# Kernel tuning notes

Measured on AMD Instinct MI355X. Metric: run time of the kernel, lower is better.

Reference implementation:

```python
import jax, jax.numpy as jnp
import numpy as np
from functools import partial

B, T, P, W = 32, 4096, 512, 128
NMEL, FILT, PDIM, K = 80, 256, 64, 9
PAD = (K - 1) // 2  # original uses (kernel[0][0]-1)//2 for both convs
EPS = 1e-5


def setup_inputs() -> dict:
    key = jax.random.key(0)
    ks = jax.random.split(key, 8)
    inp = {}
    inp["mask"] = jnp.zeros((B, P), dtype=bool)
    inp["mels"] = jax.random.normal(ks[0], (B, T, NMEL), dtype=jnp.float32)
    inp["mel_mask"] = jnp.zeros((B, T), dtype=bool)
    # uniform segments: 8 frames per phone (sum == T), 4 phones per word (sum == P)
    inp["durations"] = jnp.full((B, P), T // P, dtype=jnp.int32)
    inp["word_phone_len"] = jnp.full((B, W), P // W, dtype=jnp.int32)
    s1 = 1.0 / np.sqrt(NMEL * K)
    s2 = 1.0 / np.sqrt(FILT * K)
    s3 = 1.0 / np.sqrt(FILT)
    inp["conv1_w"] = jax.random.normal(ks[1], (FILT, NMEL, K), dtype=jnp.float32) * s1
    inp["conv1_b"] = jnp.zeros((FILT,), dtype=jnp.float32)
    inp["ln1_g"] = jnp.ones((FILT,), dtype=jnp.float32)
    inp["ln1_b"] = jnp.zeros((FILT,), dtype=jnp.float32)
    inp["conv2_w"] = jax.random.normal(ks[2], (FILT, FILT, K), dtype=jnp.float32) * s2
    inp["conv2_b"] = jnp.zeros((FILT,), dtype=jnp.float32)
    inp["ln2_g"] = jnp.ones((FILT,), dtype=jnp.float32)
    inp["ln2_b"] = jnp.zeros((FILT,), dtype=jnp.float32)
    inp["w1"] = jax.random.normal(ks[3], (FILT, FILT), dtype=jnp.float32) * s3
    inp["b1"] = jnp.zeros((FILT,), dtype=jnp.float32)
    inp["w2"] = jax.random.normal(ks[4], (FILT, PDIM), dtype=jnp.float32) * s3
    inp["b2"] = jnp.zeros((PDIM,), dtype=jnp.float32)
    return inp


def conv1d(x, w, b):
    # x: [B, T, Cin], w: [Cout, Cin, K] -> [B, T, Cout]
    y = jax.lax.conv_general_dilated(x.transpose(0, 2, 1), w, (1,), [(PAD, PAD)])
    return y.transpose(0, 2, 1) + b


def layernorm(x, g, b):
    m = jnp.mean(x, axis=-1, keepdims=True)
    v = jnp.mean(jnp.square(x - m), axis=-1, keepdims=True)
    return (x - m) * jax.lax.rsqrt(v + EPS) * g + b


def seg_mean(feat, lens, n_seg):
    # feat: [L, D], lens: [S] -> [n_seg, D] segment means
    bounds = jnp.cumsum(lens)
    ids = jnp.searchsorted(bounds, jnp.arange(feat.shape[0]), side="right")
    s = jax.ops.segment_sum(feat, ids, num_segments=n_seg)
    cnt = jnp.maximum(lens, 1).astype(feat.dtype)
    return s / cnt[:, None]


def expand_words(word_emb, wlens, n_out):
    # word_emb: [W, D]; scatter each word embedding across its phones -> [n_out, D]
    bounds = jnp.cumsum(wlens)
    wid = jnp.searchsorted(bounds, jnp.arange(n_out), side="right")
    return word_emb[jnp.clip(wid, 0, word_emb.shape[0] - 1)]


def reference(mask, mels, mel_mask, durations, word_phone_len,
              conv1_w, conv1_b, ln1_g, ln1_b, conv2_w, conv2_b, ln2_g, ln2_b,
              w1, b1, w2, b2):
    x = conv1d(mels, conv1_w, conv1_b)
    x = layernorm(jax.nn.relu(x), ln1_g, ln1_b)
    x = conv1d(x, conv2_w, conv2_b)
    x = layernorm(jax.nn.relu(x), ln2_g, ln2_b)  # [B, T, FILT]
    # token-wise (phone) mean pool over mel frames
    x = jax.vmap(partial(seg_mean, n_seg=P))(x, durations)  # [B, P, FILT]
    # word-level mean pool over phones
    x = jax.vmap(partial(seg_mean, n_seg=W))(x, word_phone_len)  # [B, W, FILT]
    x = jax.nn.relu(x @ w1 + b1)
    x = jax.nn.relu(x @ w2 + b2)  # [B, W, PDIM]
    # expand word embeddings back to phone level
    x = jax.vmap(partial(expand_words, n_out=P))(x, word_phone_len)  # [B, P, PDIM]
    x = jnp.where(mask[..., None], 0.0, x)
    return x
```

## Files before the change

kernel.cpp:

```cpp
#include <hip/hip_runtime.h>
#include <hip/hip_fp16.h>
#include <stdint.h>

#define B_ 32
#define T_ 4096
#define P_ 512
#define W_ 128
#define NMEL 80
#define FILT 256
#define PDIM 64
#define KW 9
#define TP8 (T_ + 8)
#define MSTR 104
#define YSTR 264
#define EPS 1e-5f

typedef unsigned short u16;
typedef __attribute__((ext_vector_type(8))) short short8;
typedef __attribute__((ext_vector_type(8))) _Float16 half8;
typedef __attribute__((ext_vector_type(4))) float f32x4;
typedef __attribute__((ext_vector_type(16))) float f32x16;

typedef const __attribute__((address_space(1))) uint32_t* gptr_t;
typedef __attribute__((address_space(3))) uint32_t* lptr_t;

__device__ __forceinline__ u16 f2h(float v){ return __half_as_ushort(__float2half(v)); }

#define MFMA32(accv, av, bv) \
  accv = __builtin_amdgcn_mfma_f32_32x32x16_f16((av), (bv), (accv), 0, 0, 0)

#define MFMASET(A, Bv) { \
  MFMA32(acc[0][0][0], A[0][0], Bv[0][0]); MFMA32(acc[0][0][1], A[0][0], Bv[0][1]); \
  MFMA32(acc[0][1][0], A[1][0], Bv[0][0]); MFMA32(acc[0][1][1], A[1][0], Bv[0][1]); \
  MFMA32(acc[1][0][0], A[2][0], Bv[0][0]); MFMA32(acc[1][0][1], A[2][0], Bv[0][1]); \
  MFMA32(acc[1][1][0], A[3][0], Bv[0][0]); MFMA32(acc[1][1][1], A[3][0], Bv[0][1]); \
  MFMA32(acc[0][0][0], A[0][1], Bv[1][0]); MFMA32(acc[0][0][1], A[0][1], Bv[1][1]); \
  MFMA32(acc[0][1][0], A[1][1], Bv[1][0]); MFMA32(acc[0][1][1], A[1][1], Bv[1][1]); \
  MFMA32(acc[1][0][0], A[2][1], Bv[1][0]); MFMA32(acc[1][0][1], A[2][1], Bv[1][1]); \
  MFMA32(acc[1][1][0], A[3][1], Bv[1][0]); MFMA32(acc[1][1][1], A[3][1], Bv[1][1]); }

__global__ void pack_w(const float* __restrict__ w1, const float* __restrict__ w2,
                       u16* __restrict__ Wp1, u16* __restrict__ Wp2){
  int i = blockIdx.x * 256 + threadIdx.x;
  const int N1 = KW * 12 * FILT;
  const int N2 = KW * 32 * FILT;
  if (i < N1){
    int tap = i / (12*FILT); int r = i - tap*12*FILT; int kg = r / FILT; int co = r - kg*FILT;
    short8 v;
    #pragma unroll
    for (int e=0;e<8;e++){
      int ci = kg*8 + e;
      float x = (ci < NMEL) ? w1[(co*NMEL + ci)*KW + tap] : 0.f;
      v[e] = (short)f2h(x);
    }
    *(short8*)(Wp1 + (size_t)i*8) = v;
  } else if (i < N1 + N2){
    int j = i - N1;
    int tap = j / (32*FILT); int r = j - tap*32*FILT; int kg = r / FILT; int co = r - kg*FILT;
    short8 v;
    #pragma unroll
    for (int e=0;e<8;e++){
      int ci = kg*8 + e;
      v[e] = (short)f2h(w2[(co*FILT + ci)*KW + tap]);
    }
    *(short8*)(Wp2 + (size_t)j*8) = v;
  }
}

__global__ void prep_mels(const float* __restrict__ mels, u16* __restrict__ melsPad){
  int idx = blockIdx.x * 256 + threadIdx.x;
  if (idx >= B_*TP8*13) return;
  int ch = idx % 13; int r = idx / 13; int row = r % TP8; int b = r / TP8;
  int t = row - 4;
  short8 v = (short8){0,0,0,0,0,0,0,0};
  if (t >= 0 && t < T_ && ch < 10){
    const float* src = mels + ((size_t)b*T_ + t)*NMEL + ch*8;
    const f32x4 f0 = *(const f32x4*)src;
    const f32x4 f1 = *(const f32x4*)(src+4);
    #pragma unroll
    for (int j=0;j<4;j++){ v[j]=(short)f2h(f0[j]); v[4+j]=(short)f2h(f1[j]); }
  }
  *(short8*)(melsPad + (size_t)idx*8) = v;
}

__global__ void prep_seg(const int* __restrict__ dur, const int* __restrict__ wpl,
                         int* __restrict__ wcum,
                         int* __restrict__ pid, int* __restrict__ wid,
                         u16* __restrict__ y1Pad){
  int b = blockIdx.x; int tid = threadIdx.x;
  __shared__ int dc[P_];
  __shared__ int wc[W_];
  for (int p=tid; p<P_; p+=256) dc[p] = dur[b*P_+p];
  if (tid < W_) wc[tid] = wpl[b*W_+tid];
  __syncthreads();
  if (tid == 0){ int run=0; for (int p=0;p<P_;p++){ run += dc[p]; dc[p]=run; } }
  if (tid == 64){ int run=0; for (int w=0;w<W_;w++){ run += wc[w]; wc[w]=run; wcum[b*W_+w]=run; } }
  __syncthreads();
  for (int t=tid; t<T_; t+=256){
    int lo=0, hi=P_;
    while (lo < hi){ int mid=(lo+hi)>>1; if (dc[mid] > t) hi=mid; else lo=mid+1; }
    pid[b*T_+t] = lo;
  }
  for (int p=tid; p<P_; p+=256){
    int lo=0, hi=W_;
    while (lo < hi){ int mid=(lo+hi)>>1; if (wc[mid] > p) hi=mid; else lo=mid+1; }
    wid[b*P_+p] = min(lo, W_-1);
  }
  for (int i=tid; i<8*YSTR; i+=256){
    int rr = i / YSTR; int cc = i - rr*YSTR;
    int row = (rr < 4) ? rr : (T_ + rr);
    y1Pad[((size_t)b*TP8 + row)*YSTR + cc] = 0;
  }
}

__global__ __launch_bounds__(256, 2) void conv1_k(
    const u16* __restrict__ melsPad, const u16* __restrict__ Wp1,
    const float* __restrict__ bias, const float* __restrict__ lng,
    const float* __restrict__ lnb, u16* __restrict__ y1Pad){
  __shared__ __align__(16) u16 sA[14144];
  __shared__ float sred[512], sred2[512], smean[128], srstd[128];
  const int tid = threadIdx.x;
  const int cg = tid >> 6, lane = tid & 63, l31 = lane & 31, h = lane >> 5;
  const int b = blockIdx.y, t0 = blockIdx.x * 128;

  float bcol[2], gcol[2], btcol[2];
  #pragma unroll
  for (int n=0;n<2;n++){
    int c = cg*64 + n*32 + l31;
    bcol[n]=bias[c]; gcol[n]=lng[c]; btcol[n]=lnb[c];
  }

  {
    const char* gA = (const char*)(melsPad + ((size_t)b*TP8 + t0)*MSTR);
    #pragma unroll
    for (int it=0; it<7; ++it)
      if (it*4096 + tid*16 < 28288)
        __builtin_amdgcn_global_load_lds((gptr_t)(gA + it*4096 + (cg<<10) + (lane<<4)),
                                         (lptr_t)((char*)sA + it*4096 + (cg<<10)), 16, 0, 0);
  }

  const char* gB = (const char*)Wp1 + h*4096 + cg*1024 + (l31<<4);
#define LOADB1(cc, D) { const char* nb_ = gB + (size_t)(cc)*16384; \
    D[0][0]=*(const half8*)(nb_);      D[0][1]=*(const half8*)(nb_+512); \
    D[1][0]=*(const half8*)(nb_+8192); D[1][1]=*(const half8*)(nb_+8704); }
#define LOADA1(cc, A) { const int tap_=(cc)/3, s_=(cc)%3; \
    const u16* pA_ = sA + (l31 + tap_)*MSTR + s_*32 + h*8; \
    A[0][0]=*(const half8*)(pA_);             A[0][1]=*(const half8*)(pA_+16); \
    A[1][0]=*(const half8*)(pA_+32*MSTR);     A[1][1]=*(const half8*)(pA_+32*MSTR+16); \
    A[2][0]=*(const half8*)(pA_+64*MSTR);     A[2][1]=*(const half8*)(pA_+64*MSTR+16); \
    A[3][0]=*(const half8*)(pA_+96*MSTR);     A[3][1]=*(const half8*)(pA_+96*MSTR+16); }

  half8 B0[2][2], B1[2][2], A0[4][2], A1[4][2];
  LOADB1(0, B0)
  __syncthreads();
  LOADA1(0, A0)

  f32x16 acc[2][2][2] = {};

  #pragma unroll 1
  for (int c2=0; c2<13; ++c2){
    const int cc = 2*c2;
    LOADA1(cc+1, A1) LOADB1(cc+1, B1)
    MFMASET(A0, B0)
    LOADA1(cc+2, A0) LOADB1(cc+2, B0)
    MFMASET(A1, B1)
  }
  MFMASET(A0, B0)

  #pragma unroll
  for (int st=0;st<2;++st)
    #pragma unroll
    for (int rb=0;rb<2;++rb)
      #pragma unroll
      for (int r=0;r<16;++r){
        float v0 = fmaxf(acc[st][rb][0][r] + bcol[0], 0.f);
        float v1 = fmaxf(acc[st][rb][1][r] + bcol[1], 0.f);
        float s = v0+v1, q = v0*v0+v1*v1;
        #pragma unroll
        for (int off=1; off<32; off<<=1){ s += __shfl_xor(s, off); q += __shfl_xor(q, off); }
        if (l31 == 0){ int row = st*64 + rb*32 + (r&3) + 8*(r>>2) + 4*h;
          sred[row*4+cg]=s; sred2[row*4+cg]=q; }
      }
  __syncthreads();
  if (tid < 128){
    float ss=0.f, qq=0.f;
    #pragma unroll
    for (int w2=0; w2<4; w2++){ ss += sred[tid*4+w2]; qq += sred2[tid*4+w2]; }
    float mean = ss * (1.f/FILT);
    float var  = qq * (1.f/FILT) - mean*mean;
    smean[tid] = mean;
    srstd[tid] = rsqrtf(fmaxf(var, 0.f) + EPS);
  }
  __syncthreads();

  #pragma unroll
  for (int st=0;st<2;++st)
    #pragma unroll
    for (int rb=0;rb<2;++rb)
      #pragma unroll
      for (int q=0;q<4;++q){
        const int rbase = st*64 + rb*32 + q*8 + 4*h;
        float mn0=smean[rbase+0],mn1=smean[rbase+1],mn2=smean[rbase+2],mn3=smean[rbase+3];
        float rs0=srstd[rbase+0],rs1=srstd[rbase+1],rs2=srstd[rbase+2],rs3=srstd[rbase+3];
        #pragma unroll
        for (int cb=0;cb<2;++cb){
          int c = cg*64 + cb*32 + l31;
          float x0 = fmaxf(acc[st][rb][cb][q*4+0] + bcol[cb], 0.f);
          float x1 = fmaxf(acc[st][rb][cb][q*4+1] + bcol[cb], 0.f);
          float x2 = fmaxf(acc[st][rb][cb][q*4+2] + bcol[cb], 0.f);
          float x3 = fmaxf(acc[st][rb][cb][q*4+3] + bcol[cb], 0.f);
          u16* dst = y1Pad + ((size_t)b*TP8 + 4 + t0 + rbase)*YSTR + c;
          dst[0*YSTR] = f2h((x0-mn0)*rs0*gcol[cb]+btcol[cb]);
          dst[1*YSTR] = f2h((x1-mn1)*rs1*gcol[cb]+btcol[cb]);
          dst[2*YSTR] = f2h((x2-mn2)*rs2*gcol[cb]+btcol[cb]);
          dst[3*YSTR] = f2h((x3-mn3)*rs3*gcol[cb]+btcol[cb]);
        }
      }
}

__global__ __launch_bounds__(256, 2) void conv2_k(
    const u16* __restrict__ y1Pad, const u16* __restrict__ Wp2,
    const float* __restrict__ bias, const float* __restrict__ lng,
    const float* __restrict__ lnb, const int* __restrict__ pid,
    float* __restrict__ ps){
  __shared__ __align__(16) u16 sA[35904];
  __shared__ float sred[512], sred2[512], smean[128], srstd[128];
  __shared__ int pidT[128];
  const int tid = threadIdx.x;
  const int cg = tid >> 6, lane = tid & 63, l31 = lane & 31, h = lane >> 5;
  const int b = blockIdx.y, t0 = blockIdx.x * 128;

  float bcol[2], gcol[2], btcol[2];
  #pragma unroll
  for (int n=0;n<2;n++){
    int c = cg*64 + n*32 + l31;
    bcol[n]=bias[c]; gcol[n]=lng[c]; btcol[n]=lnb[c];
  }
  if (tid < 128) pidT[tid] = pid[b*T_ + t0 + tid];

  {
    const char* gA = (const char*)(y1Pad + ((size_t)b*TP8 + t0)*YSTR);
    #pragma unroll
    for (int it=0; it<18; ++it)
      if (it*4096 + tid*16 < 71808)
        __builtin_amdgcn_global_load_lds((gptr_t)(gA + it*4096 + (cg<<10) + (lane<<4)),
                                         (lptr_t)((char*)sA + it*4096 + (cg<<10)), 16, 0, 0);
  }

  const char* gB = (const char*)Wp2 + h*4096 + cg*1024 + (l31<<4);
#define LOADB2(cc, D) { const char* nb_ = gB + (size_t)(cc)*16384; \
    D[0][0]=*(const half8*)(nb_);      D[0][1]=*(const half8*)(nb_+512); \
    D[1][0]=*(const half8*)(nb_+8192); D[1][1]=*(const half8*)(nb_+8704); }
#define LOADA2(cc, A) { const int tap_=(cc)>>3, sg_=(cc)&7; \
    const u16* pA_ = sA + (l31 + tap_)*YSTR + sg_*32 + h*8; \
    A[0][0]=*(const half8*)(pA_);             A[0][1]=*(const half8*)(pA_+16); \
    A[1][0]=*(const half8*)(pA_+32*YSTR);     A[1][1]=*(const half8*)(pA_+32*YSTR+16); \
    A[2][0]=*(const half8*)(pA_+64*YSTR);     A[2][1]=*(const half8*)(pA_+64*YSTR+16); \
    A[3][0]=*(const half8*)(pA_+96*YSTR);     A[3][1]=*(const half8*)(pA_+96*YSTR+16); }

  half8 B0[2][2], B1[2][2], A0[4][2], A1[4][2];
  LOADB2(0, B0)
  __syncthreads();
  LOADA2(0, A0)

  f32x16 acc[2][2][2] = {};

  #pragma unroll 1
  for (int c2=0; c2<36; ++c2){
    const int cc = 2*c2;
    LOADA2(cc+1, A1) LOADB2(cc+1, B1)
    MFMASET(A0, B0)
    if (c2 < 35){ LOADA2(cc+2, A0) LOADB2(cc+2, B0) }
    MFMASET(A1, B1)
  }

  #pragma unroll
  for (int st=0;st<2;++st)
    #pragma unroll
    for (int rb=0;rb<2;++rb)
      #pragma unroll
      for (int r=0;r<16;++r){
        float v0 = fmaxf(acc[st][rb][0][r] + bcol[0], 0.f);
        float v1 = fmaxf(acc[st][rb][1][r] + bcol[1], 0.f);
        float s = v0+v1, q = v0*v0+v1*v1;
        #pragma unroll
        for (int off=1; off<32; off<<=1){ s += __shfl_xor(s, off); q += __shfl_xor(q, off); }
        if (l31 == 0){ int row = st*64 + rb*32 + (r&3) + 8*(r>>2) + 4*h;
          sred[row*4+cg]=s; sred2[row*4+cg]=q; }
      }
  __syncthreads();
  if (tid < 128){
    float ss=0.f, qq=0.f;
    #pragma unroll
    for (int w2=0; w2<4; w2++){ ss += sred[tid*4+w2]; qq += sred2[tid*4+w2]; }
    float mean = ss * (1.f/FILT);
    float var  = qq * (1.f/FILT) - mean*mean;
    smean[tid] = mean;
    srstd[tid] = rsqrtf(fmaxf(var, 0.f) + EPS);
  }
  __syncthreads();

  #pragma unroll
  for (int st=0;st<2;++st)
    #pragma unroll
    for (int rb=0;rb<2;++rb)
      #pragma unroll
      for (int q=0;q<4;++q){
        const int rbase = st*64 + rb*32 + q*8 + 4*h;
        int p0v = pidT[rbase]; int fold = (p0v == pidT[rbase+3]);
        float mn0=smean[rbase+0],mn1=smean[rbase+1],mn2=smean[rbase+2],mn3=smean[rbase+3];
        float rs0=srstd[rbase+0],rs1=srstd[rbase+1],rs2=srstd[rbase+2],rs3=srstd[rbase+3];
        int pp = __shfl_xor(p0v, 32); int fp = __shfl_xor(fold, 32);
        #pragma unroll
        for (int cb=0;cb<2;++cb){
          int c = cg*64 + cb*32 + l31;
          float x0 = fmaxf(acc[st][rb][cb][q*4+0] + bcol[cb], 0.f);
          float x1 = fmaxf(acc[st][rb][cb][q*4+1] + bcol[cb], 0.f);
          float x2 = fmaxf(acc[st][rb][cb][q*4+2] + bcol[cb], 0.f);
          float x3 = fmaxf(acc[st][rb][cb][q*4+3] + bcol[cb], 0.f);
          float o0 = (x0-mn0)*rs0*gcol[cb]+btcol[cb];
          float o1 = (x1-mn1)*rs1*gcol[cb]+btcol[cb];
          float o2 = (x2-mn2)*rs2*gcol[cb]+btcol[cb];
          float o3 = (x3-mn3)*rs3*gcol[cb]+btcol[cb];
          float s4 = fold ? (o0+o1+o2+o3) : 0.f;
          float sp = __shfl_xor(s4, 32);
          float* basep = ps + (size_t)b*P_*FILT;
          if (fold){
            if (p0v < P_){
              if (fp && pp == p0v){ if (h == 0) atomicAdd(basep + (size_t)p0v*FILT + c, s4 + sp); }
              else atomicAdd(basep + (size_t)p0v*FILT + c, s4);
            }
          } else {
            int pj;
            pj = pidT[rbase+0]; if (pj < P_) atomicAdd(basep + (size_t)pj*FILT + c, o0);
            pj = pidT[rbase+1]; if (pj < P_) atomicAdd(basep + (size_t)pj*FILT + c, o1);
            pj = pidT[rbase+2]; if (pj < P_) atomicAdd(basep + (size_t)pj*FILT + c, o2);
            pj = pidT[rbase+3]; if (pj < P_) atomicAdd(basep + (size_t)pj*FILT + c, o3);
          }
        }
      }
}

#define WPB 8
__global__ __launch_bounds__(256) void word_k(
    const float* __restrict__ ps, const int* __restrict__ dur,
    const int* __restrict__ wcum, const int* __restrict__ wpl,
    const float* __restrict__ w1, const float* __restrict__ b1,
    const float* __restrict__ w2, const float* __restrict__ b2,
    float* __restrict__ wemb){
  int b = blockIdx.y, wg = blockIdx.x * WPB, tid = threadIdx.x;
  __shared__ float wvS[WPB][FILT];
  __shared__ float h1S[WPB][FILT];
  #pragma unroll
  for (int k=0;k<WPB;k++){
    int w = wg + k;
    int p1 = wcum[b*W_ + w]; int p0 = (w == 0) ? 0 : wcum[b*W_ + w - 1];
    if (p1 > P_) p1 = P_;
    int len = wpl[b*W_ + w];
    float a = 0.f;
    for (int p = p0; p < p1; ++p){
      int d = dur[b*P_ + p]; d = d < 1 ? 1 : d;
      a += ps[((size_t)(b*P_ + p))*FILT + tid] / (float)d;
    }
    wvS[k][tid] = a / (float)(len < 1 ? 1 : len);
  }
  __syncthreads();
  float acc[WPB];
  #pragma unroll
  for (int k=0;k<WPB;k++) acc[k] = b1[tid];
  for (int i=0;i<FILT;i++){
    float wcol = w1[i*FILT + tid];
    #pragma unroll
    for (int k=0;k<WPB;k++) acc[k] += wvS[k][i] * wcol;
  }
  #pragma unroll
  for (int k=0;k<WPB;k++) h1S[k][tid] = fmaxf(acc[k], 0.f);
  __syncthreads();
  int c = tid & 63, kq = tid >> 6;
  #pragma unroll
  for (int kk=kq; kk<WPB; kk+=4){
    float u = b2[c];
    for (int i=0;i<FILT;i++) u += h1S[kk][i] * w2[i*PDIM + c];
    wemb[((size_t)(b*W_ + wg + kk))*PDIM + c] = fmaxf(u, 0.f);
  }
}

__global__ void expand_k(const float* __restrict__ wemb, const int* __restrict__ wid,
                         const unsigned char* __restrict__ mask, float* __restrict__ out){
  int idx = blockIdx.x * 256 + threadIdx.x;
  if (idx >= B_*P_*16) return;
  int q = idx & 15; int p = (idx >> 4) & 511; int bb = idx >> 13;
  int w = wid[bb*P_ + p];
  f32x4 v = *(const f32x4*)(wemb + ((size_t)(bb*W_ + w))*PDIM + q*4);
  if (mask[bb*P_ + p]) v = (f32x4){0.f,0.f,0.f,0.f};
  *(f32x4*)(out + (size_t)idx*4) = v;
}

extern "C" void kernel_launch(void* const* d_in, const int* in_sizes, int n_in,
                              void* d_out, int out_size, void* d_ws, size_t ws_size,
                              hipStream_t stream) {
  const unsigned char* mask = (const unsigned char*)d_in[0];
  const float* mels = (const float*)d_in[1];
  const int*   dur  = (const int*)d_in[3];
  const int*   wpl  = (const int*)d_in[4];
  const float* c1w  = (const float*)d_in[5];
  const float* c1b  = (const float*)d_in[6];
  const float* l1g  = (const float*)d_in[7];
  const float* l1b  = (const float*)d_in[8];
  const float* c2w  = (const float*)d_in[9];
  const float* c2b  = (const float*)d_in[10];
  const float* l2g  = (const float*)d_in[11];
  const float* l2b  = (const float*)d_in[12];
  const float* w1   = (const float*)d_in[13];
  const float* b1   = (const float*)d_in[14];
  const float* w2   = (const float*)d_in[15];
  const float* b2   = (const float*)d_in[16];

  char* ws = (char*)d_ws;
  size_t off = 0;
  auto alloc = [&](size_t bytes){ void* p = ws + off; off += (bytes + 255) & ~(size_t)255; return p; };
  u16* melsPad = (u16*)alloc((size_t)B_*TP8*MSTR*2 + 32768);
  u16* y1Pad   = (u16*)alloc((size_t)B_*TP8*YSTR*2 + 32768);
  u16* Wp1     = (u16*)alloc((size_t)KW*12*FILT*8*2 + 32768);
  u16* Wp2     = (u16*)alloc((size_t)KW*32*FILT*8*2 + 32768);
  int* wcum    = (int*)alloc((size_t)B_*W_*4);
  int* pid     = (int*)alloc((size_t)B_*T_*4);
  int* wid     = (int*)alloc((size_t)B_*P_*4);
  float* psum  = (float*)alloc((size_t)B_*P_*FILT*4);
  float* wemb  = (float*)alloc((size_t)B_*W_*PDIM*4);

  hipMemsetAsync(psum, 0, (size_t)B_*P_*FILT*4, stream);
  pack_w<<<(KW*12*FILT + KW*32*FILT + 255)/256, 256, 0, stream>>>(c1w, c2w, Wp1, Wp2);
  prep_mels<<<(B_*TP8*13 + 255)/256, 256, 0, stream>>>(mels, melsPad);
  prep_seg<<<B_, 256, 0, stream>>>(dur, wpl, wcum, pid, wid, y1Pad);
  conv1_k<<<dim3(T_/128, B_), 256, 0, stream>>>(melsPad, Wp1, c1b, l1g, l1b, y1Pad);
  conv2_k<<<dim3(T_/128, B_), 256, 0, stream>>>(y1Pad, Wp2, c2b, l2g, l2b, pid, psum);
  word_k<<<dim3(W_/WPB, B_), 256, 0, stream>>>(psum, dur, wcum, wpl, w1, b1, w2, b2, wemb);
  expand_k<<<(B_*P_*16 + 255)/256, 256, 0, stream>>>(wemb, wid, mask, (float*)d_out);
}
```

Measured before the change: 349.3 us.

## Split conv tiles across eight waves and drop explicit register double-buffering

Both conv kernels now launch 512 threads, with waves arranged as 2 row groups × 4 column groups. Each wave computes a 64×64 tile instead of 128×64, halving its accumulator count. The manual A/B register ping-pong prefetch is replaced by a simple loop that relies on more resident waves to hide latency. In exchange, B weight fragments are loaded twice from global memory (once per row group). The new launch bounds request 4 blocks per CU, which may cap VGPRs tightly enough to cause spills, and LDS use in conv2 may not actually allow that many blocks.

```diff
diff --git a/kernel.cpp b/kernel.cpp
--- a/kernel.cpp
+++ b/kernel.cpp
@@ -29,16 +29,6 @@
 #define MFMA32(accv, av, bv) \
   accv = __builtin_amdgcn_mfma_f32_32x32x16_f16((av), (bv), (accv), 0, 0, 0)
 
-#define MFMASET(A, Bv) { \
-  MFMA32(acc[0][0][0], A[0][0], Bv[0][0]); MFMA32(acc[0][0][1], A[0][0], Bv[0][1]); \
-  MFMA32(acc[0][1][0], A[1][0], Bv[0][0]); MFMA32(acc[0][1][1], A[1][0], Bv[0][1]); \
-  MFMA32(acc[1][0][0], A[2][0], Bv[0][0]); MFMA32(acc[1][0][1], A[2][0], Bv[0][1]); \
-  MFMA32(acc[1][1][0], A[3][0], Bv[0][0]); MFMA32(acc[1][1][1], A[3][0], Bv[0][1]); \
-  MFMA32(acc[0][0][0], A[0][1], Bv[1][0]); MFMA32(acc[0][0][1], A[0][1], Bv[1][1]); \
-  MFMA32(acc[0][1][0], A[1][1], Bv[1][0]); MFMA32(acc[0][1][1], A[1][1], Bv[1][1]); \
-  MFMA32(acc[1][0][0], A[2][1], Bv[1][0]); MFMA32(acc[1][0][1], A[2][1], Bv[1][1]); \
-  MFMA32(acc[1][1][0], A[3][1], Bv[1][0]); MFMA32(acc[1][1][1], A[3][1], Bv[1][1]); }
-
 __global__ void pack_w(const float* __restrict__ w1, const float* __restrict__ w2,
                        u16* __restrict__ Wp1, u16* __restrict__ Wp2){
   int i = blockIdx.x * 256 + threadIdx.x;
@@ -113,14 +103,15 @@
   }
 }
 
-__global__ __launch_bounds__(256, 2) void conv1_k(
+__global__ __launch_bounds__(512, 4) void conv1_k(
     const u16* __restrict__ melsPad, const u16* __restrict__ Wp1,
     const float* __restrict__ bias, const float* __restrict__ lng,
     const float* __restrict__ lnb, u16* __restrict__ y1Pad){
   __shared__ __align__(16) u16 sA[14144];
   __shared__ float sred[512], sred2[512], smean[128], srstd[128];
   const int tid = threadIdx.x;
-  const int cg = tid >> 6, lane = tid & 63, l31 = lane & 31, h = lane >> 5;
+  const int wave = tid >> 6, lane = tid & 63, l31 = lane & 31, h = lane >> 5;
+  const int rg = wave >> 2, cg = wave & 3;
   const int b = blockIdx.y, t0 = blockIdx.x * 128;
 
   float bcol[2], gcol[2], btcol[2];
@@ -133,54 +124,47 @@
   {
     const char* gA = (const char*)(melsPad + ((size_t)b*TP8 + t0)*MSTR);
     #pragma unroll
-    for (int it=0; it<7; ++it)
-      if (it*4096 + tid*16 < 28288)
-        __builtin_amdgcn_global_load_lds((gptr_t)(gA + it*4096 + (cg<<10) + (lane<<4)),
-                                         (lptr_t)((char*)sA + it*4096 + (cg<<10)), 16, 0, 0);
-  }
-
+    for (int it=0; it<4; ++it)
+      if (it*8192 + tid*16 < 28288)
+        __builtin_amdgcn_global_load_lds((gptr_t)(gA + it*8192 + (wave<<10) + (lane<<4)),
+                                         (lptr_t)((char*)sA + it*8192 + (wave<<10)), 16, 0, 0);
+  }
   const char* gB = (const char*)Wp1 + h*4096 + cg*1024 + (l31<<4);
-#define LOADB1(cc, D) { const char* nb_ = gB + (size_t)(cc)*16384; \
-    D[0][0]=*(const half8*)(nb_);      D[0][1]=*(const half8*)(nb_+512); \
-    D[1][0]=*(const half8*)(nb_+8192); D[1][1]=*(const half8*)(nb_+8704); }
-#define LOADA1(cc, A) { const int tap_=(cc)/3, s_=(cc)%3; \
-    const u16* pA_ = sA + (l31 + tap_)*MSTR + s_*32 + h*8; \
-    A[0][0]=*(const half8*)(pA_);             A[0][1]=*(const half8*)(pA_+16); \
-    A[1][0]=*(const half8*)(pA_+32*MSTR);     A[1][1]=*(const half8*)(pA_+32*MSTR+16); \
-    A[2][0]=*(const half8*)(pA_+64*MSTR);     A[2][1]=*(const half8*)(pA_+64*MSTR+16); \
-    A[3][0]=*(const half8*)(pA_+96*MSTR);     A[3][1]=*(const half8*)(pA_+96*MSTR+16); }
-
-  half8 B0[2][2], B1[2][2], A0[4][2], A1[4][2];
-  LOADB1(0, B0)
-  __syncthreads();
-  LOADA1(0, A0)
-
-  f32x16 acc[2][2][2] = {};
-
-  #pragma unroll 1
-  for (int c2=0; c2<13; ++c2){
-    const int cc = 2*c2;
-    LOADA1(cc+1, A1) LOADB1(cc+1, B1)
-    MFMASET(A0, B0)
-    LOADA1(cc+2, A0) LOADB1(cc+2, B0)
-    MFMASET(A1, B1)
-  }
-  MFMASET(A0, B0)
-
-  #pragma unroll
-  for (int st=0;st<2;++st)
-    #pragma unroll
-    for (int rb=0;rb<2;++rb)
+  __syncthreads();
+
+  f32x16 acc[2][2] = {};
+
+  #pragma unroll 2
+  for (int cc=0; cc<27; ++cc){
+    const int tap = cc/3, s = cc - tap*3;
+    const u16* pA = sA + ((size_t)(rg*64 + l31 + tap))*MSTR + s*32 + h*8;
+    half8 a00 = *(const half8*)(pA);
+    half8 a01 = *(const half8*)(pA + 16);
+    half8 a10 = *(const half8*)(pA + 32*MSTR);
+    half8 a11 = *(const half8*)(pA + 32*MSTR + 16);
+    const char* nb = gB + (size_t)cc*16384;
+    half8 b00 = *(const half8*)(nb);
+    half8 b01 = *(const half8*)(nb + 512);
+    half8 b10 = *(const half8*)(nb + 8192);
+    half8 b11 = *(const half8*)(nb + 8704);
+    MFMA32(acc[0][0], a00, b00); MFMA32(acc[0][1], a00, b01);
+    MFMA32(acc[1][0], a10, b00); MFMA32(acc[1][1], a10, b01);
+    MFMA32(acc[0][0], a01, b10); MFMA32(acc[0][1], a01, b11);
+    MFMA32(acc[1][0], a11, b10); MFMA32(acc[1][1], a11, b11);
+  }
+
+  #pragma unroll
+  for (int rb=0;rb<2;++rb)
+    #pragma unroll
+    for (int r=0;r<16;++r){
+      float v0 = fmaxf(acc[rb][0][r] + bcol[0], 0.f);
+      float v1 = fmaxf(acc[rb][1][r] + bcol[1], 0.f);
+      float s = v0+v1, q = v0*v0+v1*v1;
       #pragma unroll
-      for (int r=0;r<16;++r){
-        float v0 = fmaxf(acc[st][rb][0][r] + bcol[0], 0.f);
-        float v1 = fmaxf(acc[st][rb][1][r] + bcol[1], 0.f);
-        float s = v0+v1, q = v0*v0+v1*v1;
-        #pragma unroll
-        for (int off=1; off<32; off<<=1){ s += __shfl_xor(s, off); q += __shfl_xor(q, off); }
-        if (l31 == 0){ int row = st*64 + rb*32 + (r&3) + 8*(r>>2) + 4*h;
-          sred[row*4+cg]=s; sred2[row*4+cg]=q; }
-      }
+      for (int off=1; off<32; off<<=1){ s += __shfl_xor(s, off); q += __shfl_xor(q, off); }
+      if (l31 == 0){ int row = rg*64 + rb*32 + (r&3) + 8*(r>>2) + 4*h;
+        sred[row*4+cg]=s; sred2[row*4+cg]=q; }
+    }
   __syncthreads();
   if (tid < 128){
     float ss=0.f, qq=0.f;
@@ -194,31 +178,29 @@
   __syncthreads();
 
   #pragma unroll
-  for (int st=0;st<2;++st)
-    #pragma unroll
-    for (int rb=0;rb<2;++rb)
+  for (int rb=0;rb<2;++rb)
+    #pragma unroll
+    for (int q=0;q<4;++q){
+      const int rbase = rg*64 + rb*32 + q*8 + 4*h;
+      float mn0=smean[rbase+0],mn1=smean[rbase+1],mn2=smean[rbase+2],mn3=smean[rbase+3];
+      float rs0=srstd[rbase+0],rs1=srstd[rbase+1],rs2=srstd[rbase+2],rs3=srstd[rbase+3];
       #pragma unroll
-      for (int q=0;q<4;++q){
-        const int rbase = st*64 + rb*32 + q*8 + 4*h;
-        float mn0=smean[rbase+0],mn1=smean[rbase+1],mn2=smean[rbase+2],mn3=smean[rbase+3];
-        float rs0=srstd[rbase+0],rs1=srstd[rbase+1],rs2=srstd[rbase+2],rs3=srstd[rbase+3];
-        #pragma unroll
-        for (int cb=0;cb<2;++cb){
-          int c = cg*64 + cb*32 + l31;
-          float x0 = fmaxf(acc[st][rb][cb][q*4+0] + bcol[cb], 0.f);
-          float x1 = fmaxf(acc[st][rb][cb][q*4+1] + bcol[cb], 0.f);
-          float x2 = fmaxf(acc[st][rb][cb][q*4+2] + bcol[cb], 0.f);
-          float x3 = fmaxf(acc[st][rb][cb][q*4+3] + bcol[cb], 0.f);
-          u16* dst = y1Pad + ((size_t)b*TP8 + 4 + t0 + rbase)*YSTR + c;
-          dst[0*YSTR] = f2h((x0-mn0)*rs0*gcol[cb]+btcol[cb]);
-          dst[1*YSTR] = f2h((x1-mn1)*rs1*gcol[cb]+btcol[cb]);
-          dst[2*YSTR] = f2h((x2-mn2)*rs2*gcol[cb]+btcol[cb]);
-          dst[3*YSTR] = f2h((x3-mn3)*rs3*gcol[cb]+btcol[cb]);
-        }
+      for (int cb=0;cb<2;++cb){
+        int c = cg*64 + cb*32 + l31;
+        float x0 = fmaxf(acc[rb][cb][q*4+0] + bcol[cb], 0.f);
+        float x1 = fmaxf(acc[rb][cb][q*4+1] + bcol[cb], 0.f);
+        float x2 = fmaxf(acc[rb][cb][q*4+2] + bcol[cb], 0.f);
+        float x3 = fmaxf(acc[rb][cb][q*4+3] + bcol[cb], 0.f);
+        u16* dst = y1Pad + ((size_t)b*TP8 + 4 + t0 + rbase)*YSTR + c;
+        dst[0*YSTR] = f2h((x0-mn0)*rs0*gcol[cb]+btcol[cb]);
+        dst[1*YSTR] = f2h((x1-mn1)*rs1*gcol[cb]+btcol[cb]);
+        dst[2*YSTR] = f2h((x2-mn2)*rs2*gcol[cb]+btcol[cb]);
+        dst[3*YSTR] = f2h((x3-mn3)*rs3*gcol[cb]+btcol[cb]);
       }
-}
-
-__global__ __launch_bounds__(256, 2) void conv2_k(
+    }
+}
+
+__global__ __launch_bounds__(512, 4) void conv2_k(
     const u16* __restrict__ y1Pad, const u16* __restrict__ Wp2,
     const float* __restrict__ bias, const float* __restrict__ lng,
     const float* __restrict__ lnb, const int* __restrict__ pid,
@@ -227,7 +209,8 @@
   __shared__ float sred[512], sred2[512], smean[128], srstd[128];
   __shared__ int pidT[128];
   const int tid = threadIdx.x;
-  const int cg = tid >> 6, lane = tid & 63, l31 = lane & 31, h = lane >> 5;
+  const int wave = tid >> 6, lane = tid & 63, l31 = lane & 31, h = lane >> 5;
+  const int rg = wave >> 2, cg = wave & 3;
   const int b = blockIdx.y, t0 = blockIdx.x * 128;
 
   float bcol[2], gcol[2], btcol[2];
@@ -241,53 +224,47 @@
   {
     const char* gA = (const char*)(y1Pad + ((size_t)b*TP8 + t0)*YSTR);
     #pragma unroll
-    for (int it=0; it<18; ++it)
-      if (it*4096 + tid*16 < 71808)
-        __builtin_amdgcn_global_load_lds((gptr_t)(gA + it*4096 + (cg<<10) + (lane<<4)),
-                                         (lptr_t)((char*)sA + it*4096 + (cg<<10)), 16, 0, 0);
-  }
-
+    for (int it=0; it<9; ++it)
+      if (it*8192 + tid*16 < 71808)
+        __builtin_amdgcn_global_load_lds((gptr_t)(gA + it*8192 + (wave<<10) + (lane<<4)),
+                                         (lptr_t)((char*)sA + it*8192 + (wave<<10)), 16, 0, 0);
+  }
   const char* gB = (const char*)Wp2 + h*4096 + cg*1024 + (l31<<4);
-#define LOADB2(cc, D) { const char* nb_ = gB + (size_t)(cc)*16384; \
-    D[0][0]=*(const half8*)(nb_);      D[0][1]=*(const half8*)(nb_+512); \
-    D[1][0]=*(const half8*)(nb_+8192); D[1][1]=*(const half8*)(nb_+8704); }
-#define LOADA2(cc, A) { const int tap_=(cc)>>3, sg_=(cc)&7; \
-    const u16* pA_ = sA + (l31 + tap_)*YSTR + sg_*32 + h*8; \
-    A[0][0]=*(const half8*)(pA_);             A[0][1]=*(const half8*)(pA_+16); \
-    A[1][0]=*(const half8*)(pA_+32*YSTR);     A[1][1]=*(const half8*)(pA_+32*YSTR+16); \
-    A[2][0]=*(const half8*)(pA_+64*YSTR);     A[2][1]=*(const half8*)(pA_+64*YSTR+16); \
-    A[3][0]=*(const half8*)(pA_+96*YSTR);     A[3][1]=*(const half8*)(pA_+96*YSTR+16); }
-
-  half8 B0[2][2], B1[2][2], A0[4][2], A1[4][2];
-  LOADB2(0, B0)
-  __syncthreads();
-  LOADA2(0, A0)
-
-  f32x16 acc[2][2][2] = {};
-
-  #pragma unroll 1
-  for (int c2=0; c2<36; ++c2){
-    const int cc = 2*c2;
-    LOADA2(cc+1, A1) LOADB2(cc+1, B1)
-    MFMASET(A0, B0)
-    if (c2 < 35){ LOADA2(cc+2, A0) LOADB2(cc+2, B0) }
-    MFMASET(A1, B1)
-  }
-
-  #pragma unroll
-  for (int st=0;st<2;++st)
-    #pragma unroll
-    for (int rb=0;rb<2;++rb)
+  __syncthreads();
+
+  f32x16 acc[2][2] = {};
+
+  #pragma unroll 2
+  for (int cc=0; cc<72; ++cc){
+    const int tap = cc>>3, sg = cc&7;
+    const u16* pA = sA + ((size_t)(rg*64 + l31 + tap))*YSTR + sg*32 + h*8;
+    half8 a00 = *(const half8*)(pA);
+    half8 a01 = *(const half8*)(pA + 16);
+    half8 a10 = *(const half8*)(pA + 32*YSTR);
+    half8 a11 = *(const half8*)(pA + 32*YSTR + 16);
+    const char* nb = gB + (size_t)cc*16384;
+    half8 b00 = *(const half8*)(nb);
+    half8 b01 = *(const half8*)(nb + 512);
+    half8 b10 = *(const half8*)(nb + 8192);
+    half8 b11 = *(const half8*)(nb + 8704);
+    MFMA32(acc[0][0], a00, b00); MFMA32(acc[0][1], a00, b01);
+    MFMA32(acc[1][0], a10, b00); MFMA32(acc[1][1], a10, b01);
+    MFMA32(acc[0][0], a01, b10); MFMA32(acc[0][1], a01, b11);
+    MFMA32(acc[1][0], a11, b10); MFMA32(acc[1][1], a11, b11);
+  }
+
+  #pragma unroll
+  for (int rb=0;rb<2;++rb)
+    #pragma unroll
+    for (int r=0;r<16;++r){
+      float v0 = fmaxf(acc[rb][0][r] + bcol[0], 0.f);
+      float v1 = fmaxf(acc[rb][1][r] + bcol[1], 0.f);
+      float s = v0+v1, q = v0*v0+v1*v1;
       #pragma unroll
-      for (int r=0;r<16;++r){
-        float v0 = fmaxf(acc[st][rb][0][r] + bcol[0], 0.f);
-        float v1 = fmaxf(acc[st][rb][1][r] + bcol[1], 0.f);
-        float s = v0+v1, q = v0*v0+v1*v1;
-        #pragma unroll
-        for (int off=1; off<32; off<<=1){ s += __shfl_xor(s, off); q += __shfl_xor(q, off); }
-        if (l31 == 0){ int row = st*64 + rb*32 + (r&3) + 8*(r>>2) + 4*h;
-          sred[row*4+cg]=s; sred2[row*4+cg]=q; }
-      }
+      for (int off=1; off<32; off<<=1){ s += __shfl_xor(s, off); q += __shfl_xor(q, off); }
+      if (l31 == 0){ int row = rg*64 + rb*32 + (r&3) + 8*(r>>2) + 4*h;
+        sred[row*4+cg]=s; sred2[row*4+cg]=q; }
+    }
   __syncthreads();
   if (tid < 128){
     float ss=0.f, qq=0.f;
@@ -301,44 +278,42 @@
   __syncthreads();
 
   #pragma unroll
-  for (int st=0;st<2;++st)
-    #pragma unroll
-    for (int rb=0;rb<2;++rb)
+  for (int rb=0;rb<2;++rb)
+    #pragma unroll
+    for (int q=0;q<4;++q){
+      const int rbase = rg*64 + rb*32 + q*8 + 4*h;
+      int p0v = pidT[rbase]; int fold = (p0v == pidT[rbase+3]);
+      float mn0=smean[rbase+0],mn1=smean[rbase+1],mn2=smean[rbase+2],mn3=smean[rbase+3];
+      float rs0=srstd[rbase+0],rs1=srstd[rbase+1],rs2=srstd[rbase+2],rs3=srstd[rbase+3];
+      int pp = __shfl_xor(p0v, 32); int fp = __shfl_xor(fold, 32);
       #pragma unroll
-      for (int q=0;q<4;++q){
-        const int rbase = st*64 + rb*32 + q*8 + 4*h;
-        int p0v = pidT[rbase]; int fold = (p0v == pidT[rbase+3]);
-        float mn0=smean[rbase+0],mn1=smean[rbase+1],mn2=smean[rbase+2],mn3=smean[rbase+3];
-        float rs0=srstd[rbase+0],rs1=srstd[rbase+1],rs2=srstd[rbase+2],rs3=srstd[rbase+3];
-        int pp = __shfl_xor(p0v, 32); int fp = __shfl_xor(fold, 32);
-        #pragma unroll
-        for (int cb=0;cb<2;++cb){
-          int c = cg*64 + cb*32 + l31;
-          float x0 = fmaxf(acc[st][rb][cb][q*4+0] + bcol[cb], 0.f);
-          float x1 = fmaxf(acc[st][rb][cb][q*4+1] + bcol[cb], 0.f);
-          float x2 = fmaxf(acc[st][rb][cb][q*4+2] + bcol[cb], 0.f);
-          float x3 = fmaxf(acc[st][rb][cb][q*4+3] + bcol[cb], 0.f);
-          float o0 = (x0-mn0)*rs0*gcol[cb]+btcol[cb];
-          float o1 = (x1-mn1)*rs1*gcol[cb]+btcol[cb];
-          float o2 = (x2-mn2)*rs2*gcol[cb]+btcol[cb];
-          float o3 = (x3-mn3)*rs3*gcol[cb]+btcol[cb];
-          float s4 = fold ? (o0+o1+o2+o3) : 0.f;
-          float sp = __shfl_xor(s4, 32);
-          float* basep = ps + (size_t)b*P_*FILT;
-          if (fold){
-            if (p0v < P_){
-              if (fp && pp == p0v){ if (h == 0) atomicAdd(basep + (size_t)p0v*FILT + c, s4 + sp); }
-              else atomicAdd(basep + (size_t)p0v*FILT + c, s4);
-            }
-          } else {
-            int pj;
-            pj = pidT[rbase+0]; if (pj < P_) atomicAdd(basep + (size_t)pj*FILT + c, o0);
-            pj = pidT[rbase+1]; if (pj < P_) atomicAdd(basep + (size_t)pj*FILT + c, o1);
-            pj = pidT[rbase+2]; if (pj < P_) atomicAdd(basep + (size_t)pj*FILT + c, o2);
-            pj = pidT[rbase+3]; if (pj < P_) atomicAdd(basep + (size_t)pj*FILT + c, o3);
+      for (int cb=0;cb<2;++cb){
+        int c = cg*64 + cb*32 + l31;
+        float x0 = fmaxf(acc[rb][cb][q*4+0] + bcol[cb], 0.f);
+        float x1 = fmaxf(acc[rb][cb][q*4+1] + bcol[cb], 0.f);
+        float x2 = fmaxf(acc[rb][cb][q*4+2] + bcol[cb], 0.f);
+        float x3 = fmaxf(acc[rb][cb][q*4+3] + bcol[cb], 0.f);
+        float o0 = (x0-mn0)*rs0*gcol[cb]+btcol[cb];
+        float o1 = (x1-mn1)*rs1*gcol[cb]+btcol[cb];
+        float o2 = (x2-mn2)*rs2*gcol[cb]+btcol[cb];
+        float o3 = (x3-mn3)*rs3*gcol[cb]+btcol[cb];
+        float s4 = fold ? (o0+o1+o2+o3) : 0.f;
+        float sp = __shfl_xor(s4, 32);
+        float* basep = ps + (size_t)b*P_*FILT;
+        if (fold){
+          if (p0v < P_){
+            if (fp && pp == p0v){ if (h == 0) atomicAdd(basep + (size_t)p0v*FILT + c, s4 + sp); }
+            else atomicAdd(basep + (size_t)p0v*FILT + c, s4);
           }
+        } else {
+          int pj;
+          pj = pidT[rbase+0]; if (pj < P_) atomicAdd(basep + (size_t)pj*FILT + c, o0);
+          pj = pidT[rbase+1]; if (pj < P_) atomicAdd(basep + (size_t)pj*FILT + c, o1);
+          pj = pidT[rbase+2]; if (pj < P_) atomicAdd(basep + (size_t)pj*FILT + c, o2);
+          pj = pidT[rbase+3]; if (pj < P_) atomicAdd(basep + (size_t)pj*FILT + c, o3);
         }
       }
+    }
 }
 
 #define WPB 8
@@ -433,8 +408,8 @@
   pack_w<<<(KW*12*FILT + KW*32*FILT + 255)/256, 256, 0, stream>>>(c1w, c2w, Wp1, Wp2);
   prep_mels<<<(B_*TP8*13 + 255)/256, 256, 0, stream>>>(mels, melsPad);
   prep_seg<<<B_, 256, 0, stream>>>(dur, wpl, wcum, pid, wid, y1Pad);
-  conv1_k<<<dim3(T_/128, B_), 256, 0, stream>>>(melsPad, Wp1, c1b, l1g, l1b, y1Pad);
-  conv2_k<<<dim3(T_/128, B_), 256, 0, stream>>>(y1Pad, Wp2, c2b, l2g, l2b, pid, psum);
+  conv1_k<<<dim3(T_/128, B_), 512, 0, stream>>>(melsPad, Wp1, c1b, l1g, l1b, y1Pad);
+  conv2_k<<<dim3(T_/128, B_), 512, 0, stream>>>(y1Pad, Wp2, c2b, l2g, l2b, pid, psum);
   word_k<<<dim3(W_/WPB, B_), 256, 0, stream>>>(psum, dur, wcum, wpl, w1, b1, w2, b2, wemb);
   expand_k<<<(B_*P_*16 + 255)/256, 256, 0, stream>>>(wemb, wid, mask, (float*)d_out);
 }
```

Result: no change. 352.9 us (+1.0%).
